# Kernel tuning notes

Hardware: AMD Instinct MI355X
Metric: run time of the kernel (lower is better)

## Reference

```python
import jax, jax.numpy as jnp
import numpy as np

N = 2048        # tokens (batch*seq)
H = 4096        # hidden_size (LLaMA-7B)
I = 11008       # intermediate_size (LLaMA-7B)
QMAX = 127.0    # int8 symmetric quant range


def setup_inputs() -> dict:
    key = jax.random.key(0)
    ks = jax.random.split(key, 6)
    # pre-quantized int8 activations (stored as int32) + per-token dynamic scales
    x_q = jax.random.randint(ks[0], (N, H), -127, 128, dtype=jnp.int32)
    x_scale = jax.random.uniform(ks[1], (N,), dtype=jnp.float32) * 0.01 + 1e-4
    # fused [gate; up] int8 weight [2I, H] with per-output-channel scales
    w_gateup = jax.random.randint(ks[2], (2 * I, H), -127, 128, dtype=jnp.int32)
    w_gateup_scale = jax.random.uniform(ks[3], (2 * I,), dtype=jnp.float32) * 0.005 + 1e-4
    # down_proj int8 weight [H, I] with per-output-channel scales
    w_down = jax.random.randint(ks[4], (H, I), -127, 128, dtype=jnp.int32)
    w_down_scale = jax.random.uniform(ks[5], (H,), dtype=jnp.float32) * 0.005 + 1e-4
    return {"x_q": x_q, "x_scale": x_scale, "w_gateup": w_gateup,
            "w_gateup_scale": w_gateup_scale, "w_down": w_down,
            "w_down_scale": w_down_scale}


def reference(x_q, x_scale, w_gateup, w_gateup_scale, w_down, w_down_scale):
    acc = jnp.matmul(x_q, w_gateup.T)                      # [N, 2I] int32
    gateup = acc.astype(jnp.float32) * x_scale[:, None] * w_gateup_scale[None, :]
    # --- fused silu_and_mul + dynamic per-token requantization ---
    gate, up = jnp.split(gateup, 2, axis=-1)               # each [N, I]
    act = jax.nn.silu(gate) * up                           # [N, I]
    s2 = jnp.max(jnp.abs(act), axis=-1) / QMAX             # [N] dynamic scale
    q2 = jnp.clip(jnp.round(act / s2[:, None]), -QMAX, QMAX)  # requantized int8 (as f32)
    out = jnp.matmul(q2, w_down.T.astype(jnp.float32)) * s2[:, None] * w_down_scale[None, :]
    return out                                             # [N, H]
```

## Files before the change

### kernel.cpp

```cpp
#include <hip/hip_runtime.h>
#include <stdint.h>

typedef int i32x4 __attribute__((ext_vector_type(4)));
typedef unsigned short u16x8 __attribute__((ext_vector_type(8)));

#define N_TOK 2048
#define HID   4096
#define INTER 11008
#define TWOI  22016
#define KT1   32
#define KT2   86

#define GLD16(gp, lp) __builtin_amdgcn_global_load_lds( \
    (const __attribute__((address_space(1))) void*)(gp), \
    (__attribute__((address_space(3))) void*)(lp), 16, 0, 0)

__device__ __forceinline__ unsigned short f2bf(float f) {
  uint32_t u = __float_as_uint(f);
  uint32_t r = (u + 0x7fffu + ((u >> 16) & 1u)) >> 16;
  return (unsigned short)r;
}

__global__ __launch_bounds__(256) void pack_tiled(
    const int* __restrict__ src, uint8_t* __restrict__ dst, int K, int KT)
{
  const long u = (long)blockIdx.x * 256 + threadIdx.x;
  const long tile = u >> 10;
  const int within = (int)(u & 1023);
  const int row = within >> 3;
  const int swc = (within & 7) << 4;
  const int col = swc ^ ((row & 7) << 4);
  const long tR = tile / KT;
  const long tK = tile - tR * KT;
  const int* s = src + (tR * 128 + row) * (long)K + tK * 128 + col;
  i32x4 o;
#pragma unroll
  for (int q = 0; q < 4; ++q) {
    i32x4 w = *reinterpret_cast<const i32x4*>(s + q * 4);
    o[q] = (w[0] & 255) | ((w[1] & 255) << 8) | ((w[2] & 255) << 16)
         | ((w[3] & 255) << 24);
  }
  *reinterpret_cast<i32x4*>(dst + tile * 16384 + (long)within * 16) = o;
}

__global__ __launch_bounds__(1024) void zero_mx(float* __restrict__ mx) {
  const int i = blockIdx.x * 1024 + threadIdx.x;
  if (i < N_TOK) mx[i] = 0.0f;
}

__global__ __launch_bounds__(512, 2) void gemm1_k(
    const uint8_t* __restrict__ x8t, const uint8_t* __restrict__ wg8t,
    const float* __restrict__ xs, const float* __restrict__ wgs,
    unsigned short* __restrict__ act, float* __restrict__ mx)
{
  __shared__ uint8_t sm[131072];
  const int tid = threadIdx.x;
  const int lane = tid & 63, wid = tid >> 6;
  const int wgm = wid >> 2, wgn = wid & 3;
  const int mt = blockIdx.x, nt = blockIdx.y;
  const int r15 = lane & 15;
  const int sxo = (r15 & 7) << 4;
  const int khi = (lane >> 4) << 4;

  const uint8_t* pA0 = x8t  + ((size_t)(2 * mt)     * KT1) * 16384 + tid * 16;
  const uint8_t* pA1 = x8t  + ((size_t)(2 * mt + 1) * KT1) * 16384 + tid * 16;
  const uint8_t* pB0 = wg8t + ((size_t)nt           * KT1) * 16384 + tid * 16;
  const uint8_t* pB1 = wg8t + ((size_t)(86 + nt)    * KT1) * 16384 + tid * 16;

  const int aoff = ((wgm << 7) + r15) << 7;
  const int boff = 32768 + (((wgn << 6) + r15) << 7);

  i32x4 acc[8][4] = {};

#define STAGE1(kt, buf) do {                                   \
    uint8_t* l = sm + (buf) * 65536;                           \
    const size_t S = (size_t)(kt) * 16384;                     \
    GLD16(pA0 + S,        l + tid * 16);                       \
    GLD16(pA0 + S + 8192, l + tid * 16 + 8192);                \
    GLD16(pA1 + S,        l + tid * 16 + 16384);               \
    GLD16(pA1 + S + 8192, l + tid * 16 + 24576);               \
    GLD16(pB0 + S,        l + tid * 16 + 32768);               \
    GLD16(pB0 + S + 8192, l + tid * 16 + 40960);               \
    GLD16(pB1 + S,        l + tid * 16 + 49152);               \
    GLD16(pB1 + S + 8192, l + tid * 16 + 57344);               \
  } while (0)

  STAGE1(0, 0);
  __syncthreads();

  for (int kt = 0; kt < KT1; ++kt) {
    if (kt + 1 < KT1) STAGE1(kt + 1, (kt + 1) & 1);
    const uint8_t* bufc = sm + (kt & 1) * 65536;
#pragma unroll
    for (int kk = 0; kk < 2; ++kk) {
      const int cs = (khi + kk * 64) ^ sxo;
      i32x4 bv[4];
#pragma unroll
      for (int n = 0; n < 4; ++n)
        bv[n] = *reinterpret_cast<const i32x4*>(bufc + boff + n * 2048 + cs);
#pragma unroll
      for (int mh = 0; mh < 2; ++mh) {
        i32x4 av[4];
#pragma unroll
        for (int m = 0; m < 4; ++m)
          av[m] = *reinterpret_cast<const i32x4*>(
              bufc + aoff + (mh * 4 + m) * 2048 + cs);
        __builtin_amdgcn_s_setprio(1);
#pragma unroll
        for (int m = 0; m < 4; ++m)
#pragma unroll
          for (int n = 0; n < 4; ++n)
            acc[mh * 4 + m][n] = __builtin_amdgcn_mfma_i32_16x16x64_i8(
                av[m], bv[n], acc[mh * 4 + m][n], 0, 0, 0);
        __builtin_amdgcn_s_setprio(0);
      }
    }
    __syncthreads();
  }
#undef STAGE1

  float* gs = (float*)sm;
  const int rq = (lane >> 4) << 2;
  if (wgn < 2) {
#pragma unroll
    for (int m = 0; m < 8; ++m) {
#pragma unroll
      for (int n = 0; n < 4; ++n) {
        const int coll = (wgn << 6) + n * 16 + r15;
        const float wsc = wgs[nt * 128 + coll];
#pragma unroll
        for (int r = 0; r < 4; ++r) {
          const int rowl = (wgm << 7) + m * 16 + rq + r;
          const float g = (float)acc[m][n][r] * xs[mt * 256 + rowl] * wsc;
          gs[rowl * 128 + (coll ^ (((rowl >> 2) & 1) << 4))] = g;
        }
      }
    }
  }
  __syncthreads();
  if (wgn >= 2) {
#pragma unroll
    for (int m = 0; m < 8; ++m) {
      float am[4] = {0.f, 0.f, 0.f, 0.f};
#pragma unroll
      for (int n = 0; n < 4; ++n) {
        const int cu = ((wgn - 2) << 6) + n * 16 + r15;
        const float wsc = wgs[INTER + nt * 128 + cu];
#pragma unroll
        for (int r = 0; r < 4; ++r) {
          const int rowl = (wgm << 7) + m * 16 + rq + r;
          const int grow = mt * 256 + rowl;
          const float uv = (float)acc[m][n][r] * xs[grow] * wsc;
          const float g = gs[rowl * 128 + (cu ^ (((rowl >> 2) & 1) << 4))];
          const float a = g / (1.f + __expf(-g)) * uv;
          act[(size_t)grow * INTER + nt * 128 + cu] = f2bf(a);
          am[r] = fmaxf(am[r], __builtin_fabsf(a));
        }
      }
#pragma unroll
      for (int r = 0; r < 4; ++r) {
#pragma unroll
        for (int off = 1; off < 16; off <<= 1)
          am[r] = fmaxf(am[r], __shfl_xor(am[r], off, 64));
      }
      if (r15 == 0) {
#pragma unroll
        for (int r = 0; r < 4; ++r)
          atomicMax((int*)&mx[mt * 256 + (wgm << 7) + m * 16 + rq + r],
                    __float_as_int(am[r]));
      }
    }
  }
}

__global__ __launch_bounds__(256) void quant_k(
    const unsigned short* __restrict__ act, const float* __restrict__ mx,
    uint8_t* __restrict__ q2t)
{
  const long u = (long)blockIdx.x * 256 + threadIdx.x;
  const long tile = u >> 10;
  const int within = (int)(u & 1023);
  const int row = within >> 3;
  const int swc = (within & 7) << 4;
  const int col = swc ^ ((row & 7) << 4);
  const long tR = tile / KT2;
  const long tK = tile - tR * KT2;
  const int grow = (int)tR * 128 + row;
  const int gcol = (int)tK * 128 + col;
  const unsigned short* ap = act + (size_t)grow * INTER + gcol;
  const float inv = 127.0f / fmaxf(mx[grow], 1e-30f);
  u16x8 a0 = *reinterpret_cast<const u16x8*>(ap);
  u16x8 a1 = *reinterpret_cast<const u16x8*>(ap + 8);
  i32x4 o;
#pragma unroll
  for (int q = 0; q < 4; ++q) {
    uint32_t d = 0;
#pragma unroll
    for (int b = 0; b < 4; ++b) {
      const int j = q * 4 + b;
      uint32_t aB = (j < 8) ? a0[j] : a1[j - 8];
      float af = __uint_as_float(aB << 16);
      float r = rintf(af * inv);
      r = fminf(fmaxf(r, -127.f), 127.f);
      d |= ((uint32_t)((int)r & 255)) << (8 * b);
    }
    o[q] = (int)d;
  }
  *reinterpret_cast<i32x4*>(q2t + tile * 16384 + (long)within * 16) = o;
}

__global__ __launch_bounds__(512, 2) void gemm2_k(
    const uint8_t* __restrict__ q2t, const uint8_t* __restrict__ wd8t,
    const float* __restrict__ mx, const float* __restrict__ wds,
    float* __restrict__ out)
{
  __shared__ uint8_t sm[98304];
  const int tid = threadIdx.x;
  const int lane = tid & 63, wid = tid >> 6;
  const int wgm = wid >> 2, wgn = wid & 3;
  const int mt = blockIdx.x, nt = blockIdx.y;
  const int r15 = lane & 15;
  const int sxo = (r15 & 7) << 4;
  const int khi = (lane >> 4) << 4;

  const uint8_t* pA  = q2t  + ((size_t)mt           * KT2) * 16384 + tid * 16;
  const uint8_t* pB0 = wd8t + ((size_t)(2 * nt)     * KT2) * 16384 + tid * 16;
  const uint8_t* pB1 = wd8t + ((size_t)(2 * nt + 1) * KT2) * 16384 + tid * 16;

  const int aoff = ((wgm << 6) + r15) << 7;
  const int boff = 16384 + (((wgn << 6) + r15) << 7);

  i32x4 acc[4][4] = {};

#define STAGE2(kt, buf) do {                                   \
    uint8_t* l = sm + (buf) * 49152;                           \
    const size_t S = (size_t)(kt) * 16384;                     \
    GLD16(pA  + S,        l + tid * 16);                       \
    GLD16(pA  + S + 8192, l + tid * 16 + 8192);                \
    GLD16(pB0 + S,        l + tid * 16 + 16384);               \
    GLD16(pB0 + S + 8192, l + tid * 16 + 24576);               \
    GLD16(pB1 + S,        l + tid * 16 + 32768);               \
    GLD16(pB1 + S + 8192, l + tid * 16 + 40960);               \
  } while (0)

  STAGE2(0, 0);
  __syncthreads();

  for (int kt = 0; kt < KT2; ++kt) {
    if (kt + 1 < KT2) STAGE2(kt + 1, (kt + 1) & 1);
    const uint8_t* bufc = sm + (kt & 1) * 49152;
#pragma unroll
    for (int kk = 0; kk < 2; ++kk) {
      const int cs = (khi + kk * 64) ^ sxo;
      i32x4 av[4], bv[4];
#pragma unroll
      for (int n = 0; n < 4; ++n)
        bv[n] = *reinterpret_cast<const i32x4*>(bufc + boff + n * 2048 + cs);
#pragma unroll
      for (int m = 0; m < 4; ++m)
        av[m] = *reinterpret_cast<const i32x4*>(bufc + aoff + m * 2048 + cs);
      __builtin_amdgcn_s_setprio(1);
#pragma unroll
      for (int m = 0; m < 4; ++m)
#pragma unroll
        for (int n = 0; n < 4; ++n)
          acc[m][n] = __builtin_amdgcn_mfma_i32_16x16x64_i8(
              av[m], bv[n], acc[m][n], 0, 0, 0);
      __builtin_amdgcn_s_setprio(0);
    }
    __syncthreads();
  }
#undef STAGE2

  const int rq = (lane >> 4) << 2;
#pragma unroll
  for (int m = 0; m < 4; ++m) {
#pragma unroll
    for (int r = 0; r < 4; ++r) {
      const int rowl = (wgm << 6) + m * 16 + rq + r;
      const int grow = mt * 128 + rowl;
      const float s2 = mx[grow] * (1.0f / 127.0f);
      float* op = out + (size_t)grow * HID + nt * 256 + (wgn << 6) + r15;
      const float* wp = wds + nt * 256 + (wgn << 6) + r15;
#pragma unroll
      for (int n = 0; n < 4; ++n)
        op[n * 16] = (float)acc[m][n][r] * s2 * wp[n * 16];
    }
  }
}

extern "C" void kernel_launch(void* const* d_in, const int* in_sizes, int n_in,
                              void* d_out, int out_size, void* d_ws, size_t ws_size,
                              hipStream_t stream)
{
  const int*   x_q = (const int*)d_in[0];
  const float* xs  = (const float*)d_in[1];
  const int*   wg  = (const int*)d_in[2];
  const float* wgs = (const float*)d_in[3];
  const int*   wd  = (const int*)d_in[4];
  const float* wds = (const float*)d_in[5];
  float* out = (float*)d_out;

  uint8_t* ws = (uint8_t*)d_ws;
  uint8_t* x8t  = ws;
  uint8_t* wg8t = x8t + 8388608;
  uint8_t* wd8t = wg8t + 90177536;
  unsigned short* act = (unsigned short*)(wd8t + 45088768);
  float* mx = (float*)((uint8_t*)act + 45088768);
  uint8_t* q2t = (uint8_t*)mx + 8192;

  zero_mx<<<2, 1024, 0, stream>>>(mx);
  pack_tiled<<<2048, 256, 0, stream>>>(x_q, x8t, HID, KT1);
  pack_tiled<<<22016, 256, 0, stream>>>(wg, wg8t, HID, KT1);
  pack_tiled<<<11008, 256, 0, stream>>>(wd, wd8t, INTER, KT2);

  gemm1_k<<<dim3(8, 86), 512, 0, stream>>>(x8t, wg8t, xs, wgs, act, mx);
  quant_k<<<5504, 256, 0, stream>>>(act, mx, q2t);
  gemm2_k<<<dim3(16, 16), 512, 0, stream>>>(q2t, wd8t, mx, wds, out);
}
```

Measured before the change: 461.5 us.

## Repack operands into K-panels and deepen GEMM pipelines to four stages

Operands are repacked into contiguous 64-byte K-panels instead of swizzled 128x128 tiles. Both int8 GEMMs now use a four-buffer LDS ring, gated by explicit vmcnt waits plus a raw barrier rather than double buffering with __syncthreads. Block indices are also remapped so consecutive workgroups share weight tiles in L2. The aim is to hide global-to-LDS latency and improve cache reuse. In exchange, the XOR swizzle is gone, which may cause LDS bank conflicts, and a barrier now runs every 64 K elements instead of every 128.

```diff
diff --git a/kernel.cpp b/kernel.cpp
--- a/kernel.cpp
+++ b/kernel.cpp
@@ -8,12 +8,14 @@
 #define HID   4096
 #define INTER 11008
 #define TWOI  22016
-#define KT1   32
-#define KT2   86
+#define KS1   64
+#define KS2   172
 
 #define GLD16(gp, lp) __builtin_amdgcn_global_load_lds( \
     (const __attribute__((address_space(1))) void*)(gp), \
     (__attribute__((address_space(3))) void*)(lp), 16, 0, 0)
+#define BAR() __builtin_amdgcn_s_barrier()
+#define WVM(n) asm volatile("s_waitcnt vmcnt(" #n ")" ::: "memory")
 
 __device__ __forceinline__ unsigned short f2bf(float f) {
   uint32_t u = __float_as_uint(f);
@@ -21,18 +23,16 @@
   return (unsigned short)r;
 }
 
-__global__ __launch_bounds__(256) void pack_tiled(
-    const int* __restrict__ src, uint8_t* __restrict__ dst, int K, int KT)
-{
-  const long u = (long)blockIdx.x * 256 + threadIdx.x;
-  const long tile = u >> 10;
-  const int within = (int)(u & 1023);
-  const int row = within >> 3;
-  const int swc = (within & 7) << 4;
-  const int col = swc ^ ((row & 7) << 4);
-  const long tR = tile / KT;
-  const long tK = tile - tR * KT;
-  const int* s = src + (tR * 128 + row) * (long)K + tK * 128 + col;
+__global__ __launch_bounds__(256) void pack_panel(
+    const int* __restrict__ src, uint8_t* __restrict__ dst, int R, int K)
+{
+  const int u = blockIdx.x * 256 + threadIdx.x;
+  const int upk = R * 4;
+  const int t = u / upk;
+  const int rem = u - t * upk;
+  const int r = rem >> 2;
+  const int c0 = (rem & 3) << 4;
+  const int* s = src + (size_t)r * K + t * 64 + c0;
   i32x4 o;
 #pragma unroll
   for (int q = 0; q < 4; ++q) {
@@ -40,7 +40,7 @@
     o[q] = (w[0] & 255) | ((w[1] & 255) << 8) | ((w[2] & 255) << 16)
          | ((w[3] & 255) << 24);
   }
-  *reinterpret_cast<i32x4*>(dst + tile * 16384 + (long)within * 16) = o;
+  *reinterpret_cast<i32x4*>(dst + (size_t)u * 16) = o;
 }
 
 __global__ __launch_bounds__(1024) void zero_mx(float* __restrict__ mx) {
@@ -49,7 +49,7 @@
 }
 
 __global__ __launch_bounds__(512, 2) void gemm1_k(
-    const uint8_t* __restrict__ x8t, const uint8_t* __restrict__ wg8t,
+    const uint8_t* __restrict__ x8p, const uint8_t* __restrict__ wgp,
     const float* __restrict__ xs, const float* __restrict__ wgs,
     unsigned short* __restrict__ act, float* __restrict__ mx)
 {
@@ -57,67 +57,60 @@
   const int tid = threadIdx.x;
   const int lane = tid & 63, wid = tid >> 6;
   const int wgm = wid >> 2, wgn = wid & 3;
-  const int mt = blockIdx.x, nt = blockIdx.y;
   const int r15 = lane & 15;
-  const int sxo = (r15 & 7) << 4;
   const int khi = (lane >> 4) << 4;
 
-  const uint8_t* pA0 = x8t  + ((size_t)(2 * mt)     * KT1) * 16384 + tid * 16;
-  const uint8_t* pA1 = x8t  + ((size_t)(2 * mt + 1) * KT1) * 16384 + tid * 16;
-  const uint8_t* pB0 = wg8t + ((size_t)nt           * KT1) * 16384 + tid * 16;
-  const uint8_t* pB1 = wg8t + ((size_t)(86 + nt)    * KT1) * 16384 + tid * 16;
-
-  const int aoff = ((wgm << 7) + r15) << 7;
-  const int boff = 32768 + (((wgn << 6) + r15) << 7);
-
+  const int bid = blockIdx.x;
+  const int v = (bid & 7) * 86 + (bid >> 3);
+  const int mt = v & 7;
+  const int nt = v >> 3;
+
+  const uint8_t* pA  = x8p + (size_t)mt * 256 * 64 + tid * 16;
+  const uint8_t* pBg = wgp + (size_t)nt * 128 * 64 + tid * 16;
+  const uint8_t* pBu = wgp + ((size_t)INTER + nt * 128) * 64 + tid * 16;
+
+  const int arow = (wgm << 7) + r15;
+  const int brow = (wgn << 6) + r15;
   i32x4 acc[8][4] = {};
 
-#define STAGE1(kt, buf) do {                                   \
-    uint8_t* l = sm + (buf) * 65536;                           \
-    const size_t S = (size_t)(kt) * 16384;                     \
-    GLD16(pA0 + S,        l + tid * 16);                       \
-    GLD16(pA0 + S + 8192, l + tid * 16 + 8192);                \
-    GLD16(pA1 + S,        l + tid * 16 + 16384);               \
-    GLD16(pA1 + S + 8192, l + tid * 16 + 24576);               \
-    GLD16(pB0 + S,        l + tid * 16 + 32768);               \
-    GLD16(pB0 + S + 8192, l + tid * 16 + 40960);               \
-    GLD16(pB1 + S,        l + tid * 16 + 49152);               \
-    GLD16(pB1 + S + 8192, l + tid * 16 + 57344);               \
+#define STG1(t, s) do {                                        \
+    uint8_t* l = sm + (s) * 32768 + tid * 16;                  \
+    const uint8_t* a = pA + (size_t)(t) * 131072;              \
+    GLD16(a, l);                                               \
+    GLD16(a + 8192, l + 8192);                                 \
+    GLD16(pBg + (size_t)(t) * 1409024, l + 16384);             \
+    GLD16(pBu + (size_t)(t) * 1409024, l + 24576);             \
   } while (0)
 
-  STAGE1(0, 0);
-  __syncthreads();
-
-  for (int kt = 0; kt < KT1; ++kt) {
-    if (kt + 1 < KT1) STAGE1(kt + 1, (kt + 1) & 1);
-    const uint8_t* bufc = sm + (kt & 1) * 65536;
-#pragma unroll
-    for (int kk = 0; kk < 2; ++kk) {
-      const int cs = (khi + kk * 64) ^ sxo;
-      i32x4 bv[4];
+  STG1(0, 0); STG1(1, 1); STG1(2, 2);
+  WVM(8); BAR();
+
+  for (int t = 0; t < KS1; ++t) {
+    const int rem = KS1 - 1 - t;
+    if (rem >= 3) STG1(t + 3, (t + 3) & 3);
+    const uint8_t* b = sm + (t & 3) * 32768;
+    i32x4 bv[4], av[8];
+#pragma unroll
+    for (int n = 0; n < 4; ++n)
+      bv[n] = *reinterpret_cast<const i32x4*>(
+          b + 16384 + (brow + n * 16) * 64 + khi);
+#pragma unroll
+    for (int m = 0; m < 8; ++m)
+      av[m] = *reinterpret_cast<const i32x4*>(b + (arow + m * 16) * 64 + khi);
+    __builtin_amdgcn_s_setprio(1);
+#pragma unroll
+    for (int m = 0; m < 8; ++m)
 #pragma unroll
       for (int n = 0; n < 4; ++n)
-        bv[n] = *reinterpret_cast<const i32x4*>(bufc + boff + n * 2048 + cs);
-#pragma unroll
-      for (int mh = 0; mh < 2; ++mh) {
-        i32x4 av[4];
-#pragma unroll
-        for (int m = 0; m < 4; ++m)
-          av[m] = *reinterpret_cast<const i32x4*>(
-              bufc + aoff + (mh * 4 + m) * 2048 + cs);
-        __builtin_amdgcn_s_setprio(1);
-#pragma unroll
-        for (int m = 0; m < 4; ++m)
-#pragma unroll
-          for (int n = 0; n < 4; ++n)
-            acc[mh * 4 + m][n] = __builtin_amdgcn_mfma_i32_16x16x64_i8(
-                av[m], bv[n], acc[mh * 4 + m][n], 0, 0, 0);
-        __builtin_amdgcn_s_setprio(0);
-      }
-    }
-    __syncthreads();
-  }
-#undef STAGE1
+        acc[m][n] = __builtin_amdgcn_mfma_i32_16x16x64_i8(
+            av[m], bv[n], acc[m][n], 0, 0, 0);
+    __builtin_amdgcn_s_setprio(0);
+    if (rem >= 3)      { WVM(8); }
+    else if (rem == 2) { WVM(4); }
+    else if (rem == 1) { WVM(0); }
+    BAR();
+  }
+#undef STG1
 
   float* gs = (float*)sm;
   const int rq = (lane >> 4) << 2;
@@ -175,20 +168,15 @@
 
 __global__ __launch_bounds__(256) void quant_k(
     const unsigned short* __restrict__ act, const float* __restrict__ mx,
-    uint8_t* __restrict__ q2t)
-{
-  const long u = (long)blockIdx.x * 256 + threadIdx.x;
-  const long tile = u >> 10;
-  const int within = (int)(u & 1023);
-  const int row = within >> 3;
-  const int swc = (within & 7) << 4;
-  const int col = swc ^ ((row & 7) << 4);
-  const long tR = tile / KT2;
-  const long tK = tile - tR * KT2;
-  const int grow = (int)tR * 128 + row;
-  const int gcol = (int)tK * 128 + col;
-  const unsigned short* ap = act + (size_t)grow * INTER + gcol;
-  const float inv = 127.0f / fmaxf(mx[grow], 1e-30f);
+    uint8_t* __restrict__ q2p)
+{
+  const int u = blockIdx.x * 256 + threadIdx.x;
+  const int t = u >> 13;
+  const int rem = u & 8191;
+  const int r = rem >> 2;
+  const int c0 = (rem & 3) << 4;
+  const unsigned short* ap = act + (size_t)r * INTER + t * 64 + c0;
+  const float inv = 127.0f / fmaxf(mx[r], 1e-30f);
   u16x8 a0 = *reinterpret_cast<const u16x8*>(ap);
   u16x8 a1 = *reinterpret_cast<const u16x8*>(ap + 8);
   i32x4 o;
@@ -200,17 +188,17 @@
       const int j = q * 4 + b;
       uint32_t aB = (j < 8) ? a0[j] : a1[j - 8];
       float af = __uint_as_float(aB << 16);
-      float r = rintf(af * inv);
-      r = fminf(fmaxf(r, -127.f), 127.f);
-      d |= ((uint32_t)((int)r & 255)) << (8 * b);
+      float rr = rintf(af * inv);
+      rr = fminf(fmaxf(rr, -127.f), 127.f);
+      d |= ((uint32_t)((int)rr & 255)) << (8 * b);
     }
     o[q] = (int)d;
   }
-  *reinterpret_cast<i32x4*>(q2t + tile * 16384 + (long)within * 16) = o;
+  *reinterpret_cast<i32x4*>(q2p + (size_t)u * 16) = o;
 }
 
 __global__ __launch_bounds__(512, 2) void gemm2_k(
-    const uint8_t* __restrict__ q2t, const uint8_t* __restrict__ wd8t,
+    const uint8_t* __restrict__ q2p, const uint8_t* __restrict__ wdp,
     const float* __restrict__ mx, const float* __restrict__ wds,
     float* __restrict__ out)
 {
@@ -218,59 +206,57 @@
   const int tid = threadIdx.x;
   const int lane = tid & 63, wid = tid >> 6;
   const int wgm = wid >> 2, wgn = wid & 3;
-  const int mt = blockIdx.x, nt = blockIdx.y;
   const int r15 = lane & 15;
-  const int sxo = (r15 & 7) << 4;
   const int khi = (lane >> 4) << 4;
 
-  const uint8_t* pA  = q2t  + ((size_t)mt           * KT2) * 16384 + tid * 16;
-  const uint8_t* pB0 = wd8t + ((size_t)(2 * nt)     * KT2) * 16384 + tid * 16;
-  const uint8_t* pB1 = wd8t + ((size_t)(2 * nt + 1) * KT2) * 16384 + tid * 16;
-
-  const int aoff = ((wgm << 6) + r15) << 7;
-  const int boff = 16384 + (((wgn << 6) + r15) << 7);
-
+  const int bid = blockIdx.x;
+  const int v = (bid & 7) * 32 + (bid >> 3);
+  const int nt = v >> 4, mt = v & 15;
+
+  const uint8_t* pA = q2p + (size_t)mt * 128 * 64 + tid * 16;
+  const uint8_t* pB = wdp + (size_t)nt * 256 * 64 + tid * 16;
+
+  const int arow = (wgm << 6) + r15;
+  const int brow = (wgn << 6) + r15;
   i32x4 acc[4][4] = {};
 
-#define STAGE2(kt, buf) do {                                   \
-    uint8_t* l = sm + (buf) * 49152;                           \
-    const size_t S = (size_t)(kt) * 16384;                     \
-    GLD16(pA  + S,        l + tid * 16);                       \
-    GLD16(pA  + S + 8192, l + tid * 16 + 8192);                \
-    GLD16(pB0 + S,        l + tid * 16 + 16384);               \
-    GLD16(pB0 + S + 8192, l + tid * 16 + 24576);               \
-    GLD16(pB1 + S,        l + tid * 16 + 32768);               \
-    GLD16(pB1 + S + 8192, l + tid * 16 + 40960);               \
+#define STG2(t, s) do {                                        \
+    uint8_t* l = sm + (s) * 24576 + tid * 16;                  \
+    GLD16(pA + (size_t)(t) * 131072, l);                       \
+    const uint8_t* bb = pB + (size_t)(t) * 262144;             \
+    GLD16(bb, l + 8192);                                       \
+    GLD16(bb + 8192, l + 16384);                               \
   } while (0)
 
-  STAGE2(0, 0);
-  __syncthreads();
-
-  for (int kt = 0; kt < KT2; ++kt) {
-    if (kt + 1 < KT2) STAGE2(kt + 1, (kt + 1) & 1);
-    const uint8_t* bufc = sm + (kt & 1) * 49152;
-#pragma unroll
-    for (int kk = 0; kk < 2; ++kk) {
-      const int cs = (khi + kk * 64) ^ sxo;
-      i32x4 av[4], bv[4];
+  STG2(0, 0); STG2(1, 1); STG2(2, 2);
+  WVM(6); BAR();
+
+  for (int t = 0; t < KS2; ++t) {
+    const int rem = KS2 - 1 - t;
+    if (rem >= 3) STG2(t + 3, (t + 3) & 3);
+    const uint8_t* b = sm + (t & 3) * 24576;
+    i32x4 bv[4], av[4];
+#pragma unroll
+    for (int n = 0; n < 4; ++n)
+      bv[n] = *reinterpret_cast<const i32x4*>(
+          b + 8192 + (brow + n * 16) * 64 + khi);
+#pragma unroll
+    for (int m = 0; m < 4; ++m)
+      av[m] = *reinterpret_cast<const i32x4*>(b + (arow + m * 16) * 64 + khi);
+    __builtin_amdgcn_s_setprio(1);
+#pragma unroll
+    for (int m = 0; m < 4; ++m)
 #pragma unroll
       for (int n = 0; n < 4; ++n)
-        bv[n] = *reinterpret_cast<const i32x4*>(bufc + boff + n * 2048 + cs);
-#pragma unroll
-      for (int m = 0; m < 4; ++m)
-        av[m] = *reinterpret_cast<const i32x4*>(bufc + aoff + m * 2048 + cs);
-      __builtin_amdgcn_s_setprio(1);
-#pragma unroll
-      for (int m = 0; m < 4; ++m)
-#pragma unroll
-        for (int n = 0; n < 4; ++n)
-          acc[m][n] = __builtin_amdgcn_mfma_i32_16x16x64_i8(
-              av[m], bv[n], acc[m][n], 0, 0, 0);
-      __builtin_amdgcn_s_setprio(0);
-    }
-    __syncthreads();
-  }
-#undef STAGE2
+        acc[m][n] = __builtin_amdgcn_mfma_i32_16x16x64_i8(
+            av[m], bv[n], acc[m][n], 0, 0, 0);
+    __builtin_amdgcn_s_setprio(0);
+    if (rem >= 3)      { WVM(6); }
+    else if (rem == 2) { WVM(3); }
+    else if (rem == 1) { WVM(0); }
+    BAR();
+  }
+#undef STG2
 
   const int rq = (lane >> 4) << 2;
 #pragma unroll
@@ -302,19 +288,19 @@
   float* out = (float*)d_out;
 
   uint8_t* ws = (uint8_t*)d_ws;
-  uint8_t* x8t  = ws;
-  uint8_t* wg8t = x8t + 8388608;
-  uint8_t* wd8t = wg8t + 90177536;
-  unsigned short* act = (unsigned short*)(wd8t + 45088768);
+  uint8_t* x8p = ws;
+  uint8_t* wgp = x8p + 8388608;
+  uint8_t* wdp = wgp + 90177536;
+  unsigned short* act = (unsigned short*)(wdp + 45088768);
   float* mx = (float*)((uint8_t*)act + 45088768);
-  uint8_t* q2t = (uint8_t*)mx + 8192;
+  uint8_t* q2p = (uint8_t*)mx + 8192;
 
   zero_mx<<<2, 1024, 0, stream>>>(mx);
-  pack_tiled<<<2048, 256, 0, stream>>>(x_q, x8t, HID, KT1);
-  pack_tiled<<<22016, 256, 0, stream>>>(wg, wg8t, HID, KT1);
-  pack_tiled<<<11008, 256, 0, stream>>>(wd, wd8t, INTER, KT2);
-
-  gemm1_k<<<dim3(8, 86), 512, 0, stream>>>(x8t, wg8t, xs, wgs, act, mx);
-  quant_k<<<5504, 256, 0, stream>>>(act, mx, q2t);
-  gemm2_k<<<dim3(16, 16), 512, 0, stream>>>(q2t, wd8t, mx, wds, out);
-}
+  pack_panel<<<2048, 256, 0, stream>>>(x_q, x8p, N_TOK, HID);
+  pack_panel<<<22016, 256, 0, stream>>>(wg, wgp, TWOI, HID);
+  pack_panel<<<11008, 256, 0, stream>>>(wd, wdp, HID, INTER);
+
+  gemm1_k<<<688, 512, 0, stream>>>(x8p, wgp, xs, wgs, act, mx);
+  quant_k<<<5504, 256, 0, stream>>>(act, mx, q2p);
+  gemm2_k<<<256, 512, 0, stream>>>(q2p, wdp, mx, wds, out);
+}
```

After: 506.5 us. 9.8% more time.
